# Optimization experiments

Measured on AMD Instinct MI355X. Metric: run time of the kernel, lower is better.

The kernel has to match this reference:

```python
import jax, jax.numpy as jnp
import numpy as np

N_NODES, N_GRAPHS, N_EDGES = 40960, 1024, 163840


def setup_inputs() -> dict:
    key = jax.random.key(0)
    ks = jax.random.split(key, 40)
    w = lambda k, s: jax.random.normal(k, s, jnp.float32) * 0.05
    inp = {
        "x": jax.random.normal(ks[0], (N_NODES, 78), jnp.float32),
        "edge_index": jax.random.randint(ks[1], (2, N_EDGES), 0, N_NODES, jnp.int32),
        "batch": jnp.repeat(jnp.arange(N_GRAPHS, dtype=jnp.int32), N_NODES // N_GRAPHS),
        "target1": jax.random.normal(ks[2], (N_GRAPHS, 750, 20), jnp.float32),
        "target2": jax.random.randint(ks[3], (N_GRAPHS, 750), 0, 26, jnp.int32),
        # GCN layers
        "W1": w(ks[4], (78, 78)), "b1": jnp.zeros((78,), jnp.float32),
        "W2": w(ks[5], (78, 156)), "b2": jnp.zeros((156,), jnp.float32),
        "W3": w(ks[6], (156, 312)), "b3": jnp.zeros((312,), jnp.float32),
        "Wg1": w(ks[7], (312, 1024)), "bg1": jnp.zeros((1024,), jnp.float32),
        "Wg2": w(ks[8], (1024, 128)), "bg2": jnp.zeros((128,), jnp.float32),
        # protein branch
        "emb": w(ks[9], (26, 128)),
        "Wc2": w(ks[10], (32, 750, 8)), "bc2": jnp.zeros((32,), jnp.float32),
        "Wxt2": w(ks[11], (32 * 121, 128)), "bxt2": jnp.zeros((128,), jnp.float32),
        "Wc1": w(ks[12], (32, 750, 8)), "bc1": jnp.zeros((32,), jnp.float32),
        "Wxt1": w(ks[13], (416, 128)), "bxt1": jnp.zeros((128,), jnp.float32),
        # fusion head
        "Wf1": w(ks[14], (384, 1024)), "bf1": jnp.zeros((1024,), jnp.float32),
        "Wf2": w(ks[15], (1024, 512)), "bf2": jnp.zeros((512,), jnp.float32),
        "Wo": w(ks[16], (512, 1)), "bo": jnp.zeros((1,), jnp.float32),
    }
    return inp


def _conv1d(x, w, b):
    # x: [B, C_in, L], w: [C_out, C_in, K] -> [B, C_out, L-K+1]
    y = jax.lax.conv_general_dilated(x, w, (1,), "VALID",
                                     dimension_numbers=("NCH", "OIH", "NCH"))
    return y + b[None, :, None]


def reference(x, edge_index, batch, target1, target2,
              W1, b1, W2, b2, W3, b3, Wg1, bg1, Wg2, bg2,
              emb, Wc2, bc2, Wxt2, bxt2, Wc1, bc1, Wxt1, bxt1,
              Wf1, bf1, Wf2, bf2, Wo, bo):
    N = x.shape[0]
    loop = jnp.arange(N, dtype=edge_index.dtype)
    src = jnp.concatenate([edge_index[0], loop])  # message source j
    dst = jnp.concatenate([edge_index[1], loop])  # aggregation target i
    # symmetric GCN normalization with self-loops (degree from dst, as in PyG)
    deg = jnp.zeros((N,), x.dtype).at[dst].add(1.0)
    dinv = jax.lax.rsqrt(deg)  # deg >= 1 due to self loops
    norm = (dinv[src] * dinv[dst])[:, None]

    def gcn(h, W, b):
        m = (h @ W)[src] * norm
        return jax.ops.segment_sum(m, dst, num_segments=N) + b

    h = jax.nn.relu(gcn(x, W1, b1))
    h = jax.nn.relu(gcn(h, W2, b2))
    h = jax.nn.relu(gcn(h, W3, b3))
    # global max pool per graph
    g = jax.ops.segment_max(h, batch, num_segments=N_GRAPHS)
    g = jax.nn.relu(g @ Wg1 + bg1)
    g = g @ Wg2 + bg2  # dropout is identity at inference

    # protein branch 2: embedding -> conv1d over channels=750
    e = emb[target2]                         # [B, 750, 128]
    xt2 = _conv1d(e, Wc2, bc2)               # [B, 32, 121]
    xt2 = xt2.reshape(-1, 32 * 121) @ Wxt2 + bxt2

    # protein branch 1: raw float features
    xt1 = _conv1d(target1, Wc1, bc1)         # [B, 32, 13]
    xt1 = xt1.reshape(-1, 416) @ Wxt1 + bxt1

    xc = jnp.concatenate([g, xt1, xt2], axis=1)  # [B, 384]
    xc = jax.nn.relu(xc @ Wf1 + bf1)
    xc = jax.nn.relu(xc @ Wf2 + bf2)
    return xc @ Wo + bo
```

## Files before the change

kernel.cpp:

```cpp
#include <hip/hip_runtime.h>
#include <hip/hip_bf16.h>

#define NN 40960
#define NE 163840
#define NB 1024

typedef __attribute__((ext_vector_type(8))) short short8;
typedef __attribute__((ext_vector_type(4))) short short4v;
typedef __attribute__((ext_vector_type(4))) float floatx4;

__device__ inline unsigned short f2bf(float f) {
    union { float f; unsigned u; } v; v.f = f;
    unsigned r = v.u + 0x7fffu + ((v.u >> 16) & 1u);
    return (unsigned short)(r >> 16);
}
__device__ inline float bf2f(unsigned short s) {
    union { unsigned u; float f; } v; v.u = ((unsigned)s) << 16; return v.f;
}
__device__ inline unsigned pack2bf(float lo, float hi) {
    return (unsigned)f2bf(lo) | ((unsigned)f2bf(hi) << 16);
}

static const size_t o_dinv = 0, o_g312 = 40960, o_g1024 = 360448, o_xc = 1409024,
                    o_f1 = 1802240, o_f2 = 2850816, o_b1v = 3375104, o_b2v = 3375232,
                    o_iws = 3375360, o_bufA = 3621124, o_bufB = 16400644;

__global__ void k_hist(const int* __restrict__ dst, int* __restrict__ cnt) {
    int e = blockIdx.x * 256 + threadIdx.x;
    if (e < NE) atomicAdd(&cnt[dst[e]], 1);
}

__global__ __launch_bounds__(1024) void k_scan1(const int* __restrict__ cnt, int* __restrict__ offTmp,
                                                int* __restrict__ blockSum, float* __restrict__ dinv) {
    __shared__ int lds[1024];
    int tid = threadIdx.x;
    int i = blockIdx.x * 1024 + tid;
    int v = cnt[i];
    dinv[i] = rsqrtf((float)v + 1.0f);
    lds[tid] = v;
    __syncthreads();
    for (int s = 1; s < 1024; s <<= 1) {
        int t = (tid >= s) ? lds[tid - s] : 0;
        __syncthreads();
        lds[tid] += t;
        __syncthreads();
    }
    offTmp[i] = lds[tid] - v;
    if (tid == 1023) blockSum[blockIdx.x] = lds[1023];
}

__global__ __launch_bounds__(64) void k_scan2(const int* __restrict__ blockSum, int* __restrict__ blockOff) {
    int l = threadIdx.x;
    int s = (l < 40) ? blockSum[l] : 0;
    int orig = s;
    for (int d = 1; d < 64; d <<= 1) {
        int t = __shfl_up(s, d);
        if (l >= d) s += t;
    }
    if (l < 40) blockOff[l] = s - orig;
}

__global__ __launch_bounds__(1024) void k_scan3(int* __restrict__ off, int* __restrict__ cur,
                                                const int* __restrict__ blockOff) {
    int i = blockIdx.x * 1024 + threadIdx.x;
    int o = off[i] + blockOff[blockIdx.x];
    off[i] = o;
    cur[i] = o;
    if (i == NN - 1) off[NN] = NE;
}

__global__ __launch_bounds__(256) void k_prep_mega(
    const float* __restrict__ W1, const float* __restrict__ W2, const float* __restrict__ W3,
    const float* __restrict__ Wg1, const float* __restrict__ Wg2, const float* __restrict__ Wf1,
    const float* __restrict__ Wf2, unsigned short* __restrict__ Wt,
    const float* __restrict__ Wc2, const float* __restrict__ Wc1,
    float* __restrict__ Wc2r, float* __restrict__ Wc1r,
    const float* __restrict__ Wxt1, float* __restrict__ Btb,
    const float* __restrict__ bc1, const float* __restrict__ bxt1, float* __restrict__ b1v,
    const float* __restrict__ bc2, const float* __restrict__ Wxt2, const float* __restrict__ bxt2,
    float* __restrict__ b2v,
    const float* __restrict__ emb, float* __restrict__ T) {
    __shared__ float el[128];
    int bx = blockIdx.x, tid = threadIdx.x;
    if (bx < 3328) {
        const int cum[8]  = {0, 128, 320, 640, 1664, 1792, 2816, 3328};
        const int KP[7]   = {96, 96, 160, 320, 1024, 384, 1024};
        const int KB[7]   = {78, 78, 156, 312, 1024, 384, 1024};
        const int NNm[7]  = {78, 156, 312, 1024, 128, 1024, 512};
        const size_t OFF[7] = {0, 12288, 30720, 81920, 409600, 540672, 933888};
        int m = 0;
        while (m < 6 && bx >= cum[m + 1]) m++;
        int r = bx - cum[m];
        const float* src = (m == 0) ? W1 : (m == 1) ? W2 : (m == 2) ? W3 : (m == 3) ? Wg1
                         : (m == 4) ? Wg2 : (m == 5) ? Wf1 : Wf2;
        int kp = KP[m], kb = KB[m], nn = NNm[m];
        unsigned short* d = Wt + OFF[m] + (size_t)r * kp;
        for (int k = tid; k < kp; k += 256) {
            float v = (r < nn && k < kb) ? src[(size_t)k * nn + r] : 0.f;
            d[k] = f2bf(v);
        }
    } else if (bx < 4828) {
        int cc = bx - 3328, j = tid;
        const float* W = (cc < 750) ? Wc2 : Wc1;
        float* Wr = (cc < 750) ? Wc2r : Wc1r;
        int c = (cc < 750) ? cc : cc - 750;
        Wr[(size_t)c * 256 + j] = W[(size_t)(j >> 3) * 6000 + c * 8 + (j & 7)];
    } else if (bx < 7388) {
        int idx = (bx - 4828) * 256 + tid;
        int j = idx & 127, ok = (idx >> 7) & 255, t = idx >> 15;
        int o = ok >> 3, k = ok & 7, lpos = t - k;
        float v = (lpos >= 0 && lpos < 13) ? Wxt1[(size_t)(o * 13 + lpos) * 128 + j] : 0.f;
        Btb[(size_t)(t * 256 + ok) * 128 + j] = v;
    } else if (bx < 7452) {
        if (tid >= 128) return;
        int b = bx - 7388, j = tid;
        if (b < 32) {
            const float* p = Wxt1 + (size_t)b * 13 * 128 + j;
            float t = 0.f;
            for (int l = 0; l < 13; l++) t += p[(size_t)l * 128];
            float add = bc1[b] * t + ((b == 0) ? bxt1[j] : 0.f);
            atomicAdd(&b1v[j], add);
        } else {
            int o = b - 32;
            const float* p = Wxt2 + (size_t)o * 121 * 128 + j;
            float t = 0.f;
            for (int l = 0; l < 121; l++) t += p[(size_t)l * 128];
            float add = bc2[o] * t + ((o == 0) ? bxt2[j] : 0.f);
            atomicAdd(&b2v[j], add);
        }
    } else {
        int tb = bx - 7452;
        int v = tb >> 4, op = tb & 15;
        int o = op * 2 + (tid >> 7), j = tid & 127;
        if (tid < 128) el[j] = emb[(size_t)v * 128 + j];
        __syncthreads();
        float acc[8] = {};
        for (int l = 0; l < 121; l++) {
            float w = Wxt2[(size_t)(o * 121 + l) * 128 + j];
#pragma unroll
            for (int k = 0; k < 8; k++) acc[k] += el[l + k] * w;
        }
#pragma unroll
        for (int k = 0; k < 8; k++) T[(size_t)(v * 256 + o * 8 + k) * 128 + j] = acc[k];
    }
}

__global__ __launch_bounds__(64) void k_agg_x(const float* __restrict__ x, const float* __restrict__ dinv,
                                              const int* __restrict__ off, const int* __restrict__ srcs,
                                              unsigned* __restrict__ out) {
    int n = blockIdx.x;
    int f = threadIdx.x;
    if (f >= 48) return;
    if (f >= 39) { out[(size_t)n * 48 + f] = 0; return; }
    float di = dinv[n];
    float2 sv = *(const float2*)&x[(size_t)n * 78 + 2 * f];
    float a0 = sv.x * di * di, a1 = sv.y * di * di;
    int e0 = off[n], e1 = off[n + 1];
    int e = e0;
    for (; e + 4 <= e1; e += 4) {
        int s0 = srcs[e], s1 = srcs[e + 1], s2 = srcs[e + 2], s3 = srcs[e + 3];
        float d0 = dinv[s0] * di, d1 = dinv[s1] * di, d2 = dinv[s2] * di, d3 = dinv[s3] * di;
        float2 v0 = *(const float2*)&x[(size_t)s0 * 78 + 2 * f];
        float2 v1 = *(const float2*)&x[(size_t)s1 * 78 + 2 * f];
        float2 v2 = *(const float2*)&x[(size_t)s2 * 78 + 2 * f];
        float2 v3 = *(const float2*)&x[(size_t)s3 * 78 + 2 * f];
        a0 += v0.x * d0 + v1.x * d1 + v2.x * d2 + v3.x * d3;
        a1 += v0.y * d0 + v1.y * d1 + v2.y * d2 + v3.y * d3;
    }
    for (; e < e1; e++) {
        int s = srcs[e];
        float dd = dinv[s] * di;
        float2 v = *(const float2*)&x[(size_t)s * 78 + 2 * f];
        a0 += v.x * dd; a1 += v.y * dd;
    }
    out[(size_t)n * 48 + f] = pack2bf(a0, a1);
}

__device__ inline void d_agg16_node(int n, int f, const unsigned* __restrict__ h,
                                    const float* __restrict__ dinv, const int* __restrict__ off,
                                    const int* __restrict__ srcs, unsigned* __restrict__ out, int F2) {
    if (f >= F2) return;
    float di = dinv[n];
    unsigned s0v = h[(size_t)n * F2 + f];
    float a0 = bf2f((unsigned short)(s0v & 0xffff)) * di * di;
    float a1 = bf2f((unsigned short)(s0v >> 16)) * di * di;
    int e0 = off[n], e1 = off[n + 1];
    int e = e0;
    for (; e + 4 <= e1; e += 4) {
        int s0 = srcs[e], s1 = srcs[e + 1], s2 = srcs[e + 2], s3 = srcs[e + 3];
        float d0 = dinv[s0] * di, d1 = dinv[s1] * di, d2 = dinv[s2] * di, d3 = dinv[s3] * di;
        unsigned v0 = h[(size_t)s0 * F2 + f];
        unsigned v1 = h[(size_t)s1 * F2 + f];
        unsigned v2 = h[(size_t)s2 * F2 + f];
        unsigned v3 = h[(size_t)s3 * F2 + f];
        a0 += bf2f((unsigned short)(v0 & 0xffff)) * d0 + bf2f((unsigned short)(v1 & 0xffff)) * d1
            + bf2f((unsigned short)(v2 & 0xffff)) * d2 + bf2f((unsigned short)(v3 & 0xffff)) * d3;
        a1 += bf2f((unsigned short)(v0 >> 16)) * d0 + bf2f((unsigned short)(v1 >> 16)) * d1
            + bf2f((unsigned short)(v2 >> 16)) * d2 + bf2f((unsigned short)(v3 >> 16)) * d3;
    }
    for (; e < e1; e++) {
        int s = srcs[e];
        float dd = dinv[s] * di;
        unsigned v = h[(size_t)s * F2 + f];
        a0 += bf2f((unsigned short)(v & 0xffff)) * dd;
        a1 += bf2f((unsigned short)(v >> 16)) * dd;
    }
    out[(size_t)n * F2 + f] = pack2bf(a0, a1);
}

__global__ void k_agg16(const unsigned* __restrict__ h, const float* __restrict__ dinv,
                        const int* __restrict__ off, const int* __restrict__ srcs,
                        unsigned* __restrict__ out, int F2) {
    d_agg16_node(blockIdx.x, threadIdx.x, h, dinv, off, srcs, out, F2);
}

#define LDST 72
template <bool ABF16, bool OUTBF16, bool ATOMIC, bool RELU_OUT>
__global__ __launch_bounds__(256) void gemm_bt(const void* __restrict__ Av, const unsigned short* __restrict__ Bt,
                                               const float* __restrict__ bias, void* __restrict__ Cv,
                                               int Nn, int Npad, int Kpad, int Klim,
                                               int lda, int ldb, int ldc, int ksplit) {
    __shared__ __align__(16) unsigned short As[64 * LDST];
    __shared__ __align__(16) unsigned short Bs[64 * LDST];
    const float* Af = (const float*)Av;
    const unsigned short* A16 = (const unsigned short*)Av;
    float* Cf = (float*)Cv;
    unsigned short* C16 = (unsigned short*)Cv;
    int bn0 = blockIdx.x * 64;
    int bm0 = blockIdx.y * 64;
    int k0 = blockIdx.z * ksplit;
    int kend = k0 + ksplit; if (kend > Kpad) kend = Kpad;
    int tid = threadIdx.x;
    int w = tid >> 6, l = tid & 63, q = l >> 4, r = l & 15;
    int wr = w >> 1, wc = w & 1;

    floatx4 acc[2][2];
#pragma unroll
    for (int i = 0; i < 2; i++)
#pragma unroll
        for (int c = 0; c < 2; c++) acc[i][c] = (floatx4)0.0f;

    int mA = tid >> 2, kcA = (tid & 3) * 8;
    int nB = tid >> 2, kcB = (tid & 3) * 8;
    int gmA = bm0 + mA;
    int gnB = bn0 + nB;

    for (int kt = k0; kt < kend; kt += 32) {
        if (ABF16) {
            *(short8*)&As[mA * LDST + kcA] = *(const short8*)(A16 + (size_t)gmA * lda + kt + kcA);
        } else {
            const float* Ap = Af + (size_t)gmA * lda + kt + kcA;
            float av[8];
            if (kt + kcA + 8 <= Klim) {
#pragma unroll
                for (int j = 0; j < 4; j++) {
                    float2 p = *(const float2*)(Ap + j * 2);
                    av[j * 2] = p.x; av[j * 2 + 1] = p.y;
                }
            } else {
#pragma unroll
                for (int j = 0; j < 8; j++) av[j] = (kt + kcA + j < Klim) ? Ap[j] : 0.f;
            }
            short8 sv;
#pragma unroll
            for (int j = 0; j < 8; j++) sv[j] = (short)f2bf(av[j]);
            *(short8*)&As[mA * LDST + kcA] = sv;
        }
        *(short8*)&Bs[nB * LDST + kcB] = *(const short8*)(Bt + (size_t)gnB * ldb + kt + kcB);
        __syncthreads();
        short8 a0 = *(const short8*)&As[(wr * 32 + r) * LDST + q * 8];
        short8 a1 = *(const short8*)&As[(wr * 32 + 16 + r) * LDST + q * 8];
        short8 b0 = *(const short8*)&Bs[(wc * 32 + r) * LDST + q * 8];
        short8 b1 = *(const short8*)&Bs[(wc * 32 + 16 + r) * LDST + q * 8];
        acc[0][0] = __builtin_amdgcn_mfma_f32_16x16x32_bf16(a0, b0, acc[0][0], 0, 0, 0);
        acc[0][1] = __builtin_amdgcn_mfma_f32_16x16x32_bf16(a0, b1, acc[0][1], 0, 0, 0);
        acc[1][0] = __builtin_amdgcn_mfma_f32_16x16x32_bf16(a1, b0, acc[1][0], 0, 0, 0);
        acc[1][1] = __builtin_amdgcn_mfma_f32_16x16x32_bf16(a1, b1, acc[1][1], 0, 0, 0);
        __syncthreads();
    }

#pragma unroll
    for (int c2 = 0; c2 < 2; c2++) {
        int col = bn0 + wc * 32 + c2 * 16 + r;
        if (col >= Npad) continue;
        bool live = col < Nn;
        float bv = (bias && live) ? bias[col] : 0.f;
#pragma unroll
        for (int i = 0; i < 2; i++) {
#pragma unroll
            for (int v = 0; v < 4; v++) {
                int row = bm0 + wr * 32 + i * 16 + q * 4 + v;
                float val = live ? (acc[i][c2][v] + bv) : 0.f;
                if (RELU_OUT) val = fmaxf(val, 0.f);
                if (OUTBF16) {
                    C16[(size_t)row * ldc + col] = live ? f2bf(val) : (unsigned short)0;
                } else if (live) {
                    if (ATOMIC) atomicAdd(&Cf[(size_t)row * ldc + col], val);
                    else Cf[(size_t)row * ldc + col] = val;
                }
            }
        }
    }
}

__global__ __launch_bounds__(256) void k_fbi(
    const int* __restrict__ ei, int* __restrict__ cur, int* __restrict__ srcOut,
    const float* __restrict__ Wc2r, const float* __restrict__ T,
    const float* __restrict__ Wc1r, const float* __restrict__ Btb,
    unsigned short* __restrict__ U16, unsigned short* __restrict__ Vt16,
    float* __restrict__ xc, float* __restrict__ f2,
    const float* __restrict__ bg2, const float* __restrict__ b1v, const float* __restrict__ bf2) {
    __shared__ __align__(16) unsigned short As[64 * LDST];
    __shared__ __align__(16) unsigned short Bs[64 * LDST];
    int bx = blockIdx.x, tid = threadIdx.x;
    if (bx < 640) {
        int e = bx * 256 + tid;
        if (e >= NE) return;
        int s = ei[e], d = ei[NE + e];
        int pos = atomicAdd(&cur[d], 1);
        srcOut[pos] = s;
        return;
    }
    if (bx >= 1744) {
        int b = bx - 1744;
        for (int t = tid; t < 768; t += 256) {
            if (t < 128) xc[(size_t)b * 384 + t] = bg2[t];
            else if (t < 256) xc[(size_t)b * 384 + t] = b1v[t - 128];
            else f2[(size_t)b * 512 + t - 256] = bf2[t - 256];
        }
        return;
    }
    int v = bx - 640;
    int gx = v & 1, gy = (v >> 1) % 12, gz = (v >> 1) / 12;
    const int M = 750, Nn = 128, K = 256;
    bool om1 = gz < 26;
    const float* A = om1 ? Wc2r : Wc1r;
    const float* Bm = om1 ? (T + (size_t)gz * 32768) : (Btb + (size_t)(gz - 26) * 32768);
    unsigned short* C16 = om1 ? (U16 + (size_t)gz * 128) : Vt16;
    int ldc = om1 ? 3328 : 15360;
    int zz = gz - 26;
    int bn0 = gx * 64;
    int bm0 = gy * 64;
    int w = tid >> 6, l = tid & 63, q = l >> 4, r = l & 15;
    int wr = w >> 1, wc = w & 1;

    floatx4 acc[2][2];
#pragma unroll
    for (int i = 0; i < 2; i++)
#pragma unroll
        for (int c = 0; c < 2; c++) acc[i][c] = (floatx4)0.0f;

    int mA = tid >> 2, kcA = (tid & 3) * 8;
    int nB = tid >> 2, kcB = (tid & 3) * 8;
    int gmA = bm0 + mA;
    int gnB = bn0 + nB;

    for (int kt = 0; kt < K; kt += 32) {
        {
            float av[8];
            const float* Ap = A + (size_t)gmA * K + kt + kcA;
            if (gmA < M) {
#pragma unroll
                for (int j = 0; j < 4; j++) {
                    float2 p = *(const float2*)(Ap + j * 2);
                    av[j * 2] = p.x; av[j * 2 + 1] = p.y;
                }
            } else {
#pragma unroll
                for (int j = 0; j < 8; j++) av[j] = 0.f;
            }
            short8 sv;
#pragma unroll
            for (int j = 0; j < 8; j++) sv[j] = (short)f2bf(av[j]);
            *(short8*)&As[mA * LDST + kcA] = sv;
        }
        {
            short8 sv;
#pragma unroll
            for (int j = 0; j < 8; j++) {
                int gk = kt + kcB + j;
                float vv = (gnB < Nn) ? Bm[(size_t)gk * Nn + gnB] : 0.f;
                sv[j] = (short)f2bf(vv);
            }
            *(short8*)&Bs[nB * LDST + kcB] = sv;
        }
        __syncthreads();
        short8 a0 = *(const short8*)&As[(wr * 32 + r) * LDST + q * 8];
        short8 a1 = *(const short8*)&As[(wr * 32 + 16 + r) * LDST + q * 8];
        short8 b0 = *(const short8*)&Bs[(wc * 32 + r) * LDST + q * 8];
        short8 b1 = *(const short8*)&Bs[(wc * 32 + 16 + r) * LDST + q * 8];
        acc[0][0] = __builtin_amdgcn_mfma_f32_16x16x32_bf16(a0, b0, acc[0][0], 0, 0, 0);
        acc[0][1] = __builtin_amdgcn_mfma_f32_16x16x32_bf16(a0, b1, acc[0][1], 0, 0, 0);
        acc[1][0] = __builtin_amdgcn_mfma_f32_16x16x32_bf16(a1, b0, acc[1][0], 0, 0, 0);
        acc[1][1] = __builtin_amdgcn_mfma_f32_16x16x32_bf16(a1, b1, acc[1][1], 0, 0, 0);
        __syncthreads();
    }

#pragma unroll
    for (int c = 0; c < 2; c++) {
        int col = bn0 + wc * 32 + c * 16 + r;
        if (col >= Nn) continue;
#pragma unroll
        for (int i = 0; i < 2; i++) {
#pragma unroll
            for (int vv = 0; vv < 4; vv++) {
                int row = bm0 + wr * 32 + i * 16 + q * 4 + vv;
                if (row >= M) continue;
                if (om1) C16[(size_t)row * ldc + col] = f2bf(acc[i][c][vv]);
                else C16[(size_t)col * ldc + row * 20 + zz] = f2bf(acc[i][c][vv]);
            }
        }
    }
}

#define T1LD 40
#define T1S  48
#define T1K  320
__global__ __launch_bounds__(256) void k_t1_l1(
    const float* __restrict__ t1A, const unsigned short* __restrict__ Bt, float* __restrict__ P,
    const unsigned short* __restrict__ A16, const unsigned short* __restrict__ W1t,
    const float* __restrict__ bias, unsigned short* __restrict__ C16) {
    __shared__ __align__(16) unsigned char smem[30720];
    int bx = blockIdx.x, tid = threadIdx.x;
    if (bx < 768) {
        unsigned short* AsS = (unsigned short*)smem;
        unsigned short* BsS = (unsigned short*)smem + 5120;
        const int Klim = 15000;
        int mt = bx & 15, ks = bx >> 4;
        int bm0 = mt * 64;
        int k0 = ks * T1K;
        int w = tid >> 6, l = tid & 63, q = l >> 4, r = l & 15;
        int wr = w >> 1, wc = w & 1;

        floatx4 acc[2][4];
#pragma unroll
        for (int i = 0; i < 2; i++)
#pragma unroll
            for (int c = 0; c < 4; c++) acc[i][c] = (floatx4)0.0f;

        int ra = tid >> 3, ca = (tid & 7) * 4;
        int rb = tid >> 2, cb = (tid & 3) * 8;
        const float* Ap0 = t1A + (size_t)(bm0 + ra) * Klim + ca;
        const float* Ap1 = t1A + (size_t)(bm0 + ra + 32) * Klim + ca;
        const unsigned short* Bp0 = Bt + (size_t)rb * 15360 + cb;
        const unsigned short* Bp1 = Bt + (size_t)(rb + 64) * 15360 + cb;

        float4 aA0, aA1, aB0, aB1;
        short8 bA0, bA1, bB0, bB1;

        auto loadT = [&](int kt, float4& x0, float4& x1, short8& y0, short8& y1) {
            int c = kt + ca;
            if (c < Klim) {
                x0 = *(const float4*)(Ap0 + kt);
                x1 = *(const float4*)(Ap1 + kt);
            } else {
                x0 = make_float4(0.f, 0.f, 0.f, 0.f);
                x1 = make_float4(0.f, 0.f, 0.f, 0.f);
            }
            y0 = *(const short8*)(Bp0 + kt);
            y1 = *(const short8*)(Bp1 + kt);
        };
        auto stageW = [&](int buf, const float4& x0, const float4& x1, const short8& y0, const short8& y1) {
            short4v s0, s1;
            s0[0] = (short)f2bf(x0.x); s0[1] = (short)f2bf(x0.y); s0[2] = (short)f2bf(x0.z); s0[3] = (short)f2bf(x0.w);
            s1[0] = (short)f2bf(x1.x); s1[1] = (short)f2bf(x1.y); s1[2] = (short)f2bf(x1.z); s1[3] = (short)f2bf(x1.w);
            *(short4v*)&AsS[buf * 2560 + ra * T1LD + ca] = s0;
            *(short4v*)&AsS[buf * 2560 + (ra + 32) * T1LD + ca] = s1;
            *(short8*)&BsS[buf * 5120 + rb * T1LD + cb] = y0;
            *(short8*)&BsS[buf * 5120 + (rb + 64) * T1LD + cb] = y1;
        };
        auto compute = [&](int buf) {
            short8 a0 = *(const short8*)&AsS[buf * 2560 + (wr * 32 + r) * T1LD + q * 8];
            short8 a1 = *(const short8*)&AsS[buf * 2560 + (wr * 32 + 16 + r) * T1LD + q * 8];
            short8 b0 = *(const short8*)&BsS[buf * 5120 + (wc * 64 + r) * T1LD + q * 8];
            short8 b1 = *(const short8*)&BsS[buf * 5120 + (wc * 64 + 16 + r) * T1LD + q * 8];
            short8 b2 = *(const short8*)&BsS[buf * 5120 + (wc * 64 + 32 + r) * T1LD + q * 8];
            short8 b3 = *(const short8*)&BsS[buf * 5120 + (wc * 64 + 48 + r) * T1LD + q * 8];
            acc[0][0] = __builtin_amdgcn_mfma_f32_16x16x32_bf16(a0, b0, acc[0][0], 0, 0, 0);
            acc[0][1] = __builtin_amdgcn_mfma_f32_16x16x32_bf16(a0, b1, acc[0][1], 0, 0, 0);
            acc[0][2] = __builtin_amdgcn_mfma_f32_16x16x32_bf16(a0, b2, acc[0][2], 0, 0, 0);
            acc[0][3] = __builtin_amdgcn_mfma_f32_16x16x32_bf16(a0, b3, acc[0][3], 0, 0, 0);
            acc[1][0] = __builtin_amdgcn_mfma_f32_16x16x32_bf16(a1, b0, acc[1][0], 0, 0, 0);
            acc[1][1] = __builtin_amdgcn_mfma_f32_16x16x32_bf16(a1, b1, acc[1][1], 0, 0, 0);
            acc[1][2] = __builtin_amdgcn_mfma_f32_16x16x32_bf16(a1, b2, acc[1][2], 0, 0, 0);
            acc[1][3] = __builtin_amdgcn_mfma_f32_16x16x32_bf16(a1, b3, acc[1][3], 0, 0, 0);
        };

        loadT(k0, aA0, aA1, bA0, bA1);
        loadT(k0 + 32, aB0, aB1, bB0, bB1);
#pragma unroll
        for (int it = 0; it < T1K / 32; it += 2) {
            stageW(0, aA0, aA1, bA0, bA1);
            if (it + 2 < T1K / 32) loadT(k0 + (it + 2) * 32, aA0, aA1, bA0, bA1);
            asm volatile("s_waitcnt lgkmcnt(0)" ::: "memory");
            __builtin_amdgcn_s_barrier();
            asm volatile("" ::: "memory");
            compute(0);
            stageW(1, aB0, aB1, bB0, bB1);
            if (it + 3 < T1K / 32) loadT(k0 + (it + 3) * 32, aB0, aB1, bB0, bB1);
            asm volatile("s_waitcnt lgkmcnt(0)" ::: "memory");
            __builtin_amdgcn_s_barrier();
            asm volatile("" ::: "memory");
            compute(1);
        }

        float* Pp = P + (size_t)ks * (1024 * 128) + (size_t)bm0 * 128;
#pragma unroll
        for (int c = 0; c < 4; c++) {
            int col = wc * 64 + c * 16 + r;
#pragma unroll
            for (int i = 0; i < 2; i++) {
#pragma unroll
                for (int v = 0; v < 4; v++) {
                    int row = wr * 32 + i * 16 + q * 4 + v;
                    Pp[(size_t)row * 128 + col] = acc[i][c][v];
                }
            }
        }
    } else {
        unsigned short* As = (unsigned short*)smem;
        unsigned short* Bs = (unsigned short*)smem + 4608;
        int v = bx - 768;
        int bn0 = (v & 1) * 64;
        int bm0 = (v >> 1) * 64;
        int w = tid >> 6, l = tid & 63, q = l >> 4, r = l & 15;
        int wr = w >> 1, wc = w & 1;

        floatx4 acc[2][2];
#pragma unroll
        for (int i = 0; i < 2; i++)
#pragma unroll
            for (int c = 0; c < 2; c++) acc[i][c] = (floatx4)0.0f;

        int mA = tid >> 2, kcA = (tid & 3) * 8;
        int gmA = bm0 + mA;
        int gnB = bn0 + mA;

        for (int kt = 0; kt < 96; kt += 32) {
            *(short8*)&As[mA * LDST + kcA] = *(const short8*)(A16 + (size_t)gmA * 96 + kt + kcA);
            *(short8*)&Bs[mA * LDST + kcA] = *(const short8*)(W1t + (size_t)gnB * 96 + kt + kcA);
            __syncthreads();
            short8 a0 = *(const short8*)&As[(wr * 32 + r) * LDST + q * 8];
            short8 a1 = *(const short8*)&As[(wr * 32 + 16 + r) * LDST + q * 8];
            short8 b0 = *(const short8*)&Bs[(wc * 32 + r) * LDST + q * 8];
            short8 b1 = *(const short8*)&Bs[(wc * 32 + 16 + r) * LDST + q * 8];
            acc[0][0] = __builtin_amdgcn_mfma_f32_16x16x32_bf16(a0, b0, acc[0][0], 0, 0, 0);
            acc[0][1] = __builtin_amdgcn_mfma_f32_16x16x32_bf16(a0, b1, acc[0][1], 0, 0, 0);
            acc[1][0] = __builtin_amdgcn_mfma_f32_16x16x32_bf16(a1, b0, acc[1][0], 0, 0, 0);
            acc[1][1] = __builtin_amdgcn_mfma_f32_16x16x32_bf16(a1, b1, acc[1][1], 0, 0, 0);
            __syncthreads();
        }

#pragma unroll
        for (int c2 = 0; c2 < 2; c2++) {
            int col = bn0 + wc * 32 + c2 * 16 + r;
            if (col >= 96) continue;
            bool live = col < 78;
            float bv = live ? bias[col] : 0.f;
#pragma unroll
            for (int i = 0; i < 2; i++) {
#pragma unroll
                for (int vv = 0; vv < 4; vv++) {
                    int row = bm0 + wr * 32 + i * 16 + q * 4 + vv;
                    float val = live ? fmaxf(acc[i][c2][vv] + bv, 0.f) : 0.f;
                    C16[(size_t)row * 96 + col] = live ? f2bf(val) : (unsigned short)0;
                }
            }
        }
    }
}

__global__ __launch_bounds__(128) void k_agg16_ug(
    const unsigned* __restrict__ h, const float* __restrict__ dinv, const int* __restrict__ off,
    const int* __restrict__ srcs, unsigned* __restrict__ outb,
    const int* __restrict__ t2, const unsigned short* __restrict__ U,
    const float* __restrict__ b2v, float* __restrict__ xc) {
    __shared__ int offs[752];
    __shared__ float red[8][128];
    int bx = blockIdx.x, tid = threadIdx.x;
    if (bx < NB) {
        int b = bx;
        int rg = tid >> 4, lane = tid & 15;
        const int* t2b = t2 + (size_t)b * 750;
        for (int i = tid; i < 750; i += 128) offs[i] = i * 3328 + t2b[i] * 128;
        __syncthreads();
        float a[8] = {};
#pragma unroll 4
        for (int i = rg; i < 750; i += 8) {
            short8 v = *(const short8*)&U[(size_t)offs[i] + lane * 8];
#pragma unroll
            for (int c = 0; c < 8; c++) a[c] += bf2f((unsigned short)v[c]);
        }
#pragma unroll
        for (int c = 0; c < 8; c++) red[rg][lane * 8 + c] = a[c];
        __syncthreads();
        float s = b2v[tid];
#pragma unroll
        for (int g = 0; g < 8; g++) s += red[g][tid];
        xc[(size_t)b * 384 + 256 + tid] = s;
    } else {
        d_agg16_node(bx - NB, tid, h, dinv, off, srcs, outb, 80);
    }
}

__global__ void k_segmax_red(const unsigned short* __restrict__ h, unsigned short* __restrict__ g,
                             const float* __restrict__ P, float* __restrict__ xc) {
    int bx = blockIdx.x, tid = threadIdx.x;
    if (bx < NB) {
        if (tid < 128) {
            int row = bx, j = tid;
            const float* p = P + (size_t)row * 128 + j;
            float s = 0.f;
#pragma unroll
            for (int ks = 0; ks < T1S; ks++) s += p[(size_t)ks * (1024 * 128)];
            xc[(size_t)row * 384 + 128 + j] += s;
        }
    } else {
        int gr = bx - NB, f = tid;
        if (f >= 320) return;
        if (f >= 312) { g[(size_t)gr * 320 + f] = 0; return; }
        float m = 0.0f;
        const unsigned short* base = h + (size_t)gr * 40 * 312 + f;
        for (int i = 0; i < 40; i++) m = fmaxf(m, bf2f(base[(size_t)i * 312]));
        g[(size_t)gr * 320 + f] = f2bf(m);
    }
}

__global__ __launch_bounds__(64) void k_final(const float* __restrict__ f2, const float* __restrict__ Wo,
                                              const float* __restrict__ bo, float* __restrict__ out) {
    int b = blockIdx.x, lane = threadIdx.x;
    float s = 0.f;
    for (int j = lane; j < 512; j += 64) s += fmaxf(f2[(size_t)b * 512 + j], 0.f) * Wo[j];
    for (int off = 32; off; off >>= 1) s += __shfl_down(s, off);
    if (lane == 0) out[b] = s + bo[0];
}

extern "C" void kernel_launch(void* const* d_in, const int* in_sizes, int n_in,
                              void* d_out, int out_size, void* d_ws, size_t ws_size,
                              hipStream_t stream) {
    const float* x    = (const float*)d_in[0];
    const int*   ei   = (const int*)d_in[1];
    const float* t1   = (const float*)d_in[3];
    const int*   t2   = (const int*)d_in[4];
    const float* W1   = (const float*)d_in[5];
    const float* b1   = (const float*)d_in[6];
    const float* W2   = (const float*)d_in[7];
    const float* b2   = (const float*)d_in[8];
    const float* W3   = (const float*)d_in[9];
    const float* b3   = (const float*)d_in[10];
    const float* Wg1  = (const float*)d_in[11];
    const float* bg1  = (const float*)d_in[12];
    const float* Wg2  = (const float*)d_in[13];
    const float* bg2  = (const float*)d_in[14];
    const float* emb  = (const float*)d_in[15];
    const float* Wc2  = (const float*)d_in[16];
    const float* bc2  = (const float*)d_in[17];
    const float* Wxt2 = (const float*)d_in[18];
    const float* bxt2 = (const float*)d_in[19];
    const float* Wc1  = (const float*)d_in[20];
    const float* bc1  = (const float*)d_in[21];
    const float* Wxt1 = (const float*)d_in[22];
    const float* bxt1 = (const float*)d_in[23];
    const float* Wf1  = (const float*)d_in[24];
    const float* bf1  = (const float*)d_in[25];
    const float* Wf2  = (const float*)d_in[26];
    const float* bf2  = (const float*)d_in[27];
    const float* Wo   = (const float*)d_in[28];
    const float* bo   = (const float*)d_in[29];
    float* out = (float*)d_out;

    float* ws = (float*)d_ws;
    float* dinv  = ws + o_dinv;
    unsigned short* g312b = (unsigned short*)(ws + o_g312);
    unsigned short* g1024b = (unsigned short*)(ws + o_g1024);
    float* xc    = ws + o_xc;
    unsigned short* f1b = (unsigned short*)(ws + o_f1);
    float* f2    = ws + o_f2;
    float* b1v   = ws + o_b1v;
    float* b2v   = ws + o_b2v;
    int* csrOff  = (int*)(ws + o_iws);
    int* csrCur  = csrOff + (NN + 1);
    int* csrSrc  = csrCur + NN;
    int* blockSum = (int*)(ws + o_f1 + 600000);
    int* blockOff = blockSum + 40;
    float* bufA  = ws + o_bufA;
    float* bufB  = ws + o_bufB;
    float* T    = bufA;
    unsigned short* U16  = (unsigned short*)(bufA + 851968);
    unsigned short* Vt16 = (unsigned short*)(bufA + 2200000);
    unsigned short* Wt   = (unsigned short*)(bufA + 3200000);
    float* Wc2r = bufA + 4000000;
    float* Wc1r = bufA + 4200000;
    float* Btb  = bufA + 4400000;
    float* Pt1  = bufA + 6000000;
    unsigned* aggb = (unsigned*)bufB;
    unsigned short* h16 = (unsigned short*)(bufB + 5500000);

    unsigned short* W1t  = Wt + 0;
    unsigned short* W2t  = Wt + 12288;
    unsigned short* W3t  = Wt + 30720;
    unsigned short* Wg1t = Wt + 81920;
    unsigned short* Wg2t = Wt + 409600;
    unsigned short* Wf1t = Wt + 540672;
    unsigned short* Wf2t = Wt + 933888;

    hipMemsetAsync(Vt16, 0, (size_t)128 * 15360 * 2, stream);
    hipMemsetAsync(b1v, 0, 256 * sizeof(float), stream);
    hipMemsetAsync(csrCur, 0, NN * sizeof(int), stream);
    k_hist<<<NE / 256, 256, 0, stream>>>(ei + NE, csrCur);
    k_scan1<<<40, 1024, 0, stream>>>(csrCur, csrOff, blockSum, dinv);
    k_scan2<<<1, 64, 0, stream>>>(blockSum, blockOff);
    k_scan3<<<40, 1024, 0, stream>>>(csrOff, csrCur, blockOff);

    k_prep_mega<<<7868, 256, 0, stream>>>(W1, W2, W3, Wg1, Wg2, Wf1, Wf2, Wt,
                                          Wc2, Wc1, Wc2r, Wc1r,
                                          Wxt1, Btb, bc1, bxt1, b1v,
                                          bc2, Wxt2, bxt2, b2v, emb, T);

    k_fbi<<<2768, 256, 0, stream>>>(ei, csrCur, csrSrc, Wc2r, T, Wc1r, Btb, U16, Vt16,
                                    xc, f2, bg2, b1v, bf2);

    k_agg_x<<<NN, 64, 0, stream>>>(x, dinv, csrOff, csrSrc, aggb);

    k_t1_l1<<<2048, 256, 0, stream>>>(t1, Vt16, Pt1, (const unsigned short*)aggb, W1t, b1, h16);

    k_agg16<<<NN, 64, 0, stream>>>((unsigned*)h16, dinv, csrOff, csrSrc, aggb, 48);
    gemm_bt<true, true, false, true><<<dim3(3, 640, 1), 256, 0, stream>>>(
        aggb, W2t, b2, h16, 156, 160, 96, 96, 96, 96, 160, 96);
    k_agg16_ug<<<NB + NN, 128, 0, stream>>>((unsigned*)h16, dinv, csrOff, csrSrc, aggb,
                                            t2, U16, b2v, xc);
    gemm_bt<true, true, false, true><<<dim3(5, 640, 1), 256, 0, stream>>>(
        aggb, W3t, b3, h16, 312, 312, 160, 160, 160, 160, 312, 160);
    k_segmax_red<<<2 * NB, 320, 0, stream>>>(h16, g312b, Pt1, xc);
    gemm_bt<true, true, false, true><<<dim3(16, 16, 1), 256, 0, stream>>>(
        g312b, Wg1t, bg1, g1024b, 1024, 1024, 320, 320, 320, 320, 1024, 320);

    gemm_bt<true, false, true, false><<<dim3(2, 16, 8), 256, 0, stream>>>(
        g1024b, Wg2t, nullptr, xc + 0, 128, 128, 1024, 1024, 1024, 1024, 384, 128);

    gemm_bt<false, true, false, true><<<dim3(16, 16, 1), 256, 0, stream>>>(
        xc, Wf1t, bf1, f1b, 1024, 1024, 384, 384, 384, 384, 1024, 384);
    gemm_bt<true, false, true, false><<<dim3(8, 16, 4), 256, 0, stream>>>(
        f1b, Wf2t, nullptr, f2, 512, 512, 1024, 1024, 1024, 1024, 512, 256);
    k_final<<<NB, 64, 0, stream>>>(f2, Wo, bo, out);
}
```

Baseline: 423.3 us.

## Fuse histogram into prep kernel and merge three scan kernels into one

Folds the edge-degree histogram into the weight-prep mega kernel as extra blocks, and replaces the three-kernel scan (block scan, block-sum scan, offset add) with a single kernel in which the 40 blocks exchange totals through a global flag spin-wait. This removes four kernel launches and their serialization gaps. The inter-block spin relies on all 40 blocks being co-resident, and cnt is read and cur written in the same buffer, which is safe only because every block reads its counts before any block passes the barrier.

```diff
diff --git a/kernel.cpp b/kernel.cpp
--- a/kernel.cpp
+++ b/kernel.cpp
@@ -25,51 +25,8 @@
                     o_f1 = 1802240, o_f2 = 2850816, o_b1v = 3375104, o_b2v = 3375232,
                     o_iws = 3375360, o_bufA = 3621124, o_bufB = 16400644;
 
-__global__ void k_hist(const int* __restrict__ dst, int* __restrict__ cnt) {
-    int e = blockIdx.x * 256 + threadIdx.x;
-    if (e < NE) atomicAdd(&cnt[dst[e]], 1);
-}
-
-__global__ __launch_bounds__(1024) void k_scan1(const int* __restrict__ cnt, int* __restrict__ offTmp,
-                                                int* __restrict__ blockSum, float* __restrict__ dinv) {
-    __shared__ int lds[1024];
-    int tid = threadIdx.x;
-    int i = blockIdx.x * 1024 + tid;
-    int v = cnt[i];
-    dinv[i] = rsqrtf((float)v + 1.0f);
-    lds[tid] = v;
-    __syncthreads();
-    for (int s = 1; s < 1024; s <<= 1) {
-        int t = (tid >= s) ? lds[tid - s] : 0;
-        __syncthreads();
-        lds[tid] += t;
-        __syncthreads();
-    }
-    offTmp[i] = lds[tid] - v;
-    if (tid == 1023) blockSum[blockIdx.x] = lds[1023];
-}
-
-__global__ __launch_bounds__(64) void k_scan2(const int* __restrict__ blockSum, int* __restrict__ blockOff) {
-    int l = threadIdx.x;
-    int s = (l < 40) ? blockSum[l] : 0;
-    int orig = s;
-    for (int d = 1; d < 64; d <<= 1) {
-        int t = __shfl_up(s, d);
-        if (l >= d) s += t;
-    }
-    if (l < 40) blockOff[l] = s - orig;
-}
-
-__global__ __launch_bounds__(1024) void k_scan3(int* __restrict__ off, int* __restrict__ cur,
-                                                const int* __restrict__ blockOff) {
-    int i = blockIdx.x * 1024 + threadIdx.x;
-    int o = off[i] + blockOff[blockIdx.x];
-    off[i] = o;
-    cur[i] = o;
-    if (i == NN - 1) off[NN] = NE;
-}
-
-__global__ __launch_bounds__(256) void k_prep_mega(
+__global__ __launch_bounds__(256) void k_histprep(
+    const int* __restrict__ dst, int* __restrict__ cnt, int* __restrict__ flag,
     const float* __restrict__ W1, const float* __restrict__ W2, const float* __restrict__ W3,
     const float* __restrict__ Wg1, const float* __restrict__ Wg2, const float* __restrict__ Wf1,
     const float* __restrict__ Wf2, unsigned short* __restrict__ Wt,
@@ -82,15 +39,22 @@
     const float* __restrict__ emb, float* __restrict__ T) {
     __shared__ float el[128];
     int bx = blockIdx.x, tid = threadIdx.x;
-    if (bx < 3328) {
+    if (bx < 640) {
+        int e = bx * 256 + tid;
+        if (e < NE) atomicAdd(&cnt[dst[e]], 1);
+        return;
+    }
+    int bp = bx - 640;
+    if (bp == 0 && tid == 0) *flag = 0;
+    if (bp < 3328) {
         const int cum[8]  = {0, 128, 320, 640, 1664, 1792, 2816, 3328};
         const int KP[7]   = {96, 96, 160, 320, 1024, 384, 1024};
         const int KB[7]   = {78, 78, 156, 312, 1024, 384, 1024};
         const int NNm[7]  = {78, 156, 312, 1024, 128, 1024, 512};
         const size_t OFF[7] = {0, 12288, 30720, 81920, 409600, 540672, 933888};
         int m = 0;
-        while (m < 6 && bx >= cum[m + 1]) m++;
-        int r = bx - cum[m];
+        while (m < 6 && bp >= cum[m + 1]) m++;
+        int r = bp - cum[m];
         const float* src = (m == 0) ? W1 : (m == 1) ? W2 : (m == 2) ? W3 : (m == 3) ? Wg1
                          : (m == 4) ? Wg2 : (m == 5) ? Wf1 : Wf2;
         int kp = KP[m], kb = KB[m], nn = NNm[m];
@@ -99,21 +63,21 @@
             float v = (r < nn && k < kb) ? src[(size_t)k * nn + r] : 0.f;
             d[k] = f2bf(v);
         }
-    } else if (bx < 4828) {
-        int cc = bx - 3328, j = tid;
+    } else if (bp < 4828) {
+        int cc = bp - 3328, j = tid;
         const float* W = (cc < 750) ? Wc2 : Wc1;
         float* Wr = (cc < 750) ? Wc2r : Wc1r;
         int c = (cc < 750) ? cc : cc - 750;
         Wr[(size_t)c * 256 + j] = W[(size_t)(j >> 3) * 6000 + c * 8 + (j & 7)];
-    } else if (bx < 7388) {
-        int idx = (bx - 4828) * 256 + tid;
+    } else if (bp < 7388) {
+        int idx = (bp - 4828) * 256 + tid;
         int j = idx & 127, ok = (idx >> 7) & 255, t = idx >> 15;
         int o = ok >> 3, k = ok & 7, lpos = t - k;
         float v = (lpos >= 0 && lpos < 13) ? Wxt1[(size_t)(o * 13 + lpos) * 128 + j] : 0.f;
         Btb[(size_t)(t * 256 + ok) * 128 + j] = v;
-    } else if (bx < 7452) {
+    } else if (bp < 7452) {
         if (tid >= 128) return;
-        int b = bx - 7388, j = tid;
+        int b = bp - 7388, j = tid;
         if (b < 32) {
             const float* p = Wxt1 + (size_t)b * 13 * 128 + j;
             float t = 0.f;
@@ -129,7 +93,7 @@
             atomicAdd(&b2v[j], add);
         }
     } else {
-        int tb = bx - 7452;
+        int tb = bp - 7452;
         int v = tb >> 4, op = tb & 15;
         int o = op * 2 + (tid >> 7), j = tid & 127;
         if (tid < 128) el[j] = emb[(size_t)v * 128 + j];
@@ -143,6 +107,43 @@
 #pragma unroll
         for (int k = 0; k < 8; k++) T[(size_t)(v * 256 + o * 8 + k) * 128 + j] = acc[k];
     }
+}
+
+__global__ __launch_bounds__(1024) void k_scan_all(const int* __restrict__ cnt, int* __restrict__ off,
+                                                   int* __restrict__ cur, float* __restrict__ dinv,
+                                                   int* __restrict__ blockSum, int* __restrict__ flag) {
+    __shared__ int lds[1024];
+    __shared__ int bs[40];
+    int tid = threadIdx.x, bx = blockIdx.x;
+    int i = bx * 1024 + tid;
+    int v = cnt[i];
+    dinv[i] = rsqrtf((float)v + 1.0f);
+    lds[tid] = v;
+    __syncthreads();
+    for (int s = 1; s < 1024; s <<= 1) {
+        int t = (tid >= s) ? lds[tid - s] : 0;
+        __syncthreads();
+        lds[tid] += t;
+        __syncthreads();
+    }
+    int localExcl = lds[tid] - v;
+    if (tid == 1023) {
+        atomicExch(&blockSum[bx], lds[1023]);
+        __threadfence();
+        atomicAdd(flag, 1);
+    }
+    if (tid == 0) {
+        while (atomicAdd(flag, 0) < 40) { }
+    }
+    __syncthreads();
+    if (tid < 40) bs[tid] = atomicAdd(&blockSum[tid], 0);
+    __syncthreads();
+    int pref = 0;
+    for (int j = 0; j < bx; j++) pref += bs[j];
+    int o = localExcl + pref;
+    off[i] = o;
+    cur[i] = o;
+    if (i == NN - 1) off[NN] = NE;
 }
 
 __global__ __launch_bounds__(64) void k_agg_x(const float* __restrict__ x, const float* __restrict__ dinv,
@@ -682,7 +683,7 @@
     int* csrCur  = csrOff + (NN + 1);
     int* csrSrc  = csrCur + NN;
     int* blockSum = (int*)(ws + o_f1 + 600000);
-    int* blockOff = blockSum + 40;
+    int* scanFlag = blockSum + 63;
     float* bufA  = ws + o_bufA;
     float* bufB  = ws + o_bufB;
     float* T    = bufA;
@@ -707,15 +708,14 @@
     hipMemsetAsync(Vt16, 0, (size_t)128 * 15360 * 2, stream);
     hipMemsetAsync(b1v, 0, 256 * sizeof(float), stream);
     hipMemsetAsync(csrCur, 0, NN * sizeof(int), stream);
-    k_hist<<<NE / 256, 256, 0, stream>>>(ei + NE, csrCur);
-    k_scan1<<<40, 1024, 0, stream>>>(csrCur, csrOff, blockSum, dinv);
-    k_scan2<<<1, 64, 0, stream>>>(blockSum, blockOff);
-    k_scan3<<<40, 1024, 0, stream>>>(csrOff, csrCur, blockOff);
-
-    k_prep_mega<<<7868, 256, 0, stream>>>(W1, W2, W3, Wg1, Wg2, Wf1, Wf2, Wt,
-                                          Wc2, Wc1, Wc2r, Wc1r,
-                                          Wxt1, Btb, bc1, bxt1, b1v,
-                                          bc2, Wxt2, bxt2, b2v, emb, T);
+
+    k_histprep<<<8508, 256, 0, stream>>>(ei + NE, csrCur, scanFlag,
+                                         W1, W2, W3, Wg1, Wg2, Wf1, Wf2, Wt,
+                                         Wc2, Wc1, Wc2r, Wc1r,
+                                         Wxt1, Btb, bc1, bxt1, b1v,
+                                         bc2, Wxt2, bxt2, b2v, emb, T);
+
+    k_scan_all<<<40, 1024, 0, stream>>>(csrCur, csrOff, csrCur, dinv, blockSum, scanFlag);
 
     k_fbi<<<2768, 256, 0, stream>>>(ei, csrCur, csrSrc, Wc2r, T, Wc1r, Btb, U16, Vt16,
                                     xc, f2, bg2, b1v, bf2);
```

Result: no change. 419.9 us (-0.8%).
